# Optimization experiments

Hardware: AMD Instinct MI355X
Metric: run time of the kernel (lower is better)

## Reference

```python
import jax, jax.numpy as jnp
import numpy as np
from jax import lax

GROUPS = 8
THR = 0.5
EPS = 1e-5

def setup_inputs() -> dict:
    key = jax.random.key(0)
    ks = jax.random.split(key, 7)
    b, c, h, w = 64, 256, 1024, 1
    cg = c // GROUPS  # 32
    x = jax.random.normal(ks[0], (b, c, h, w), jnp.float32)
    w1 = jax.random.normal(ks[1], (cg, cg), jnp.float32) * 0.1     # conv1x1 weight [out,in]
    b1 = jnp.zeros((cg,), jnp.float32)
    w3 = jax.random.normal(ks[2], (cg, cg, 3, 3), jnp.float32) * 0.05  # conv3x3 OIHW
    b3 = jnp.zeros((cg,), jnp.float32)
    gamma = jnp.ones((cg,), jnp.float32)
    beta = jnp.zeros((cg,), jnp.float32)
    return {"x": x, "w1": w1, "b1": b1, "w3": w3, "b3": b3, "gamma": gamma, "beta": beta}

def reference(x, w1, b1, w3, b3, gamma, beta):
    b, c, h, w = x.shape
    g = GROUPS
    cg = c // g
    bg = b * g
    gx = x.reshape(bg, cg, h, w)

    # pool_h is AvgPool2d((1,1)) -> identity; pool_w averages over h then permutes
    x_h = gx                                               # [bg,cg,h,1]
    x_w = jnp.mean(gx, axis=2, keepdims=True).transpose(0, 1, 3, 2)  # [bg,cg,w,1]
    cat = jnp.concatenate([x_h, x_w], axis=2)              # [bg,cg,h+w,1]
    hw = jnp.einsum('oi,bihw->bohw', w1, cat) + b1[None, :, None, None]
    xh, xw = hw[:, :, :h], hw[:, :, h:]                    # [bg,cg,h,1], [bg,cg,w,1]

    gated = gx * jax.nn.sigmoid(xh) * jax.nn.sigmoid(xw.transpose(0, 1, 3, 2))
    # GroupNorm(cg, cg): normalize each channel over spatial dims, affine per channel
    mu = jnp.mean(gated, axis=(2, 3), keepdims=True)
    var = jnp.mean(jnp.square(gated - mu), axis=(2, 3), keepdims=True)
    x1 = (gated - mu) * lax.rsqrt(var + EPS) * gamma[None, :, None, None] + beta[None, :, None, None]

    x2 = lax.conv_general_dilated(gx, w3, (1, 1), ((1, 1), (1, 1)),
                                  dimension_numbers=('NCHW', 'OIHW', 'NCHW')) + b3[None, :, None, None]

    # agp: AvgPool2d((avg_len,1)) with h==avg_len, w==1 -> mean over spatial dims
    x11 = jax.nn.softmax(jnp.mean(x1, axis=(2, 3)), axis=-1)  # [bg,cg]
    x21 = jax.nn.softmax(jnp.mean(x2, axis=(2, 3)), axis=-1)  # [bg,cg]
    x12 = x2.reshape(bg, cg, h * w)
    x22 = x1.reshape(bg, cg, h * w)
    weights = (jnp.einsum('bc,bcn->bn', x11, x12) +
               jnp.einsum('bc,bcn->bn', x21, x22)).reshape(bg, 1, h, w)

    rew = gx * jax.nn.sigmoid(weights)
    info = rew >= THR
    x_1 = jnp.where(info, gx, 0.0)
    x_2 = jnp.where(info, 0.0, gx)
    half = cg // 2
    out = jnp.concatenate([x_1[:, :half] + x_2[:, half:],
                           x_1[:, half:] + x_2[:, :half]], axis=1)
    return out.reshape(b, c, h, w)
```

## Files before the change

### kernel.cpp

```cpp
#include <hip/hip_runtime.h>
#include <math.h>

#define CG   32
#define H    1024
#define NBG  512
#define CHN  8
#define BROW (H + 2)
#define EPSV 1e-5f
#define THRV 0.5f

__global__ __launch_bounds__(1024, 4)
void emaru_kernel(const float* __restrict__ x,  const float* __restrict__ w1,
                  const float* __restrict__ b1, const float* __restrict__ w3,
                  const float* __restrict__ b3, const float* __restrict__ gamma,
                  const float* __restrict__ beta, float* __restrict__ out)
{
    __shared__ float  buf[CHN][BROW];
    __shared__ float  w1s[1024];
    __shared__ float  w3s[3072];
    __shared__ double redP[CG][2];
    __shared__ double redQ[CG][2];
    __shared__ float  sigwS[CG], x11S[CG], x21S[CG], As[CG], Bs[CG], Cs[CG],
                      muS[CG], rsgS[CG], b1S[CG], b3S[CG], betaS[CG],
                      g0S[CG], gNS[CG];

    const int t  = threadIdx.x;
    const int bg = blockIdx.x;
    const long base = (long)bg * (CG * H);
    const int wid = t >> 6, lane = t & 63;

    w1s[t] = w1[t];
    #pragma unroll
    for (int r = 0; r < 3; ++r) w3s[r*1024 + t] = w3[(r*1024 + t)*3 + 1];
    if (t < CG) { b1S[t] = b1[t]; b3S[t] = b3[t]; betaS[t] = beta[t]; }

    float g[CG], gated[CG];
    #pragma unroll
    for (int c = 0; c < CG; ++c) g[c] = x[base + c*H + t];
    if (t == 0) {
        #pragma unroll
        for (int c = 0; c < CG; ++c) g0S[c] = g[c];
    }
    if (t == H-1) {
        #pragma unroll
        for (int c = 0; c < CG; ++c) gNS[c] = g[c];
    }
    __syncthreads();

    if (t < CG) {
        float m = betaS[0];
        #pragma unroll
        for (int i = 1; i < CG; ++i) m = fmaxf(m, betaS[i]);
        float s = 0.f;
        #pragma unroll
        for (int i = 0; i < CG; ++i) s += expf(betaS[i] - m);
        const float inv = 1.f / s;
        x11S[t] = expf(betaS[t] - m) * inv;
        float a = 0.f, b = 0.f, c = 0.f;
        #pragma unroll
        for (int o = 0; o < CG; ++o) {
            const float f = expf(betaS[o] - m) * inv;
            a = fmaf(f, w3s[(o*CG + t)*3 + 0], a);
            b = fmaf(f, w3s[(o*CG + t)*3 + 1], b);
            c = fmaf(f, w3s[(o*CG + t)*3 + 2], c);
        }
        As[t] = a; Bs[t] = b; Cs[t] = c;
    }

    float cd = 0.f;
    #pragma unroll
    for (int ch = 0; ch < CG/CHN; ++ch) {
        __syncthreads();
        #pragma unroll
        for (int i = 0; i < CHN; ++i) buf[i][1 + t] = g[ch*CHN + i];
        if (t < CHN) { buf[t][0] = 0.f; buf[t][1 + H] = 0.f; }
        __syncthreads();
        {
            const int cl = wid >> 1, half = wid & 1;
            const int pos = half*512 + lane;
            double acc = 0.0;
            #pragma unroll
            for (int k = 0; k < 8; ++k) acc += (double)buf[cl][1 + pos + (k << 6)];
            #pragma unroll
            for (int off = 32; off; off >>= 1) acc += __shfl_down(acc, off);
            if (lane == 0) redP[ch*CHN + cl][half] = acc;
        }
        #pragma unroll
        for (int i = 0; i < CHN; ++i) {
            const int gi = ch*CHN + i;
            cd = fmaf(As[gi], buf[i][t],     cd);
            cd = fmaf(Bs[gi], g[gi],         cd);
            cd = fmaf(Cs[gi], buf[i][2 + t], cd);
        }
    }
    __syncthreads();

    if (wid == 0 && lane < CG) {
        const int o = lane;
        float acc = b1S[o];
        for (int i = 0; i < CG; ++i) {
            const float mi = (float)((redP[i][0] + redP[i][1]) * (1.0/H));
            acc = fmaf(w1s[o*CG + i], mi, acc);
        }
        sigwS[o] = 1.f / (1.f + expf(-acc));
    } else if (wid == 1 && lane < CG) {
        const int o = lane;
        double m2 = 0.0;
        for (int i = 0; i < CG; ++i) {
            const double Si = redP[i][0] + redP[i][1];
            m2 += (double)w3s[(o*CG + i)*3 + 0] * (Si - (double)gNS[i])
                + (double)w3s[(o*CG + i)*3 + 1] * Si
                + (double)w3s[(o*CG + i)*3 + 2] * (Si - (double)g0S[i]);
        }
        float mv = (float)(m2 * (1.0/H)) + b3S[o];
        float mx = mv;
        #pragma unroll
        for (int off = 16; off; off >>= 1) mx = fmaxf(mx, __shfl_xor(mx, off));
        const float e = expf(mv - mx);
        float se = e;
        #pragma unroll
        for (int off = 16; off; off >>= 1) se += __shfl_xor(se, off);
        x21S[o] = e / se;
    }
    __syncthreads();

    #pragma unroll
    for (int o = 0; o < CG; ++o) {
        float acc = b1S[o];
        #pragma unroll
        for (int i4 = 0; i4 < CG/4; ++i4) {
            const float4 wv = *reinterpret_cast<const float4*>(&w1s[o*CG + i4*4]);
            acc = fmaf(wv.x, g[i4*4+0], acc);
            acc = fmaf(wv.y, g[i4*4+1], acc);
            acc = fmaf(wv.z, g[i4*4+2], acc);
            acc = fmaf(wv.w, g[i4*4+3], acc);
        }
        gated[o] = g[o] * (1.f / (1.f + expf(-acc))) * sigwS[o];
    }
    #pragma unroll
    for (int o = 0; o < CG; ++o) cd = fmaf(x11S[o], b3S[o], cd);

    #pragma unroll
    for (int ch = 0; ch < CG/CHN; ++ch) {
        __syncthreads();
        #pragma unroll
        for (int i = 0; i < CHN; ++i) buf[i][1 + t] = gated[ch*CHN + i];
        __syncthreads();
        const int cl = wid >> 1, half = wid & 1;
        const int pos = half*512 + lane;
        double sg = 0.0, sq = 0.0;
        #pragma unroll
        for (int k = 0; k < 8; ++k) {
            const double v = (double)buf[cl][1 + pos + (k << 6)];
            sg += v; sq = fma(v, v, sq);
        }
        #pragma unroll
        for (int off = 32; off; off >>= 1) { sg += __shfl_down(sg, off); sq += __shfl_down(sq, off); }
        if (lane == 0) { redP[ch*CHN + cl][half] = sg; redQ[ch*CHN + cl][half] = sq; }
    }
    __syncthreads();
    if (t < CG) {
        const double sg = redP[t][0] + redP[t][1];
        const double sq = redQ[t][0] + redQ[t][1];
        const double mu  = sg * (1.0/H);
        const double var = sq * (1.0/H) - mu*mu;
        muS[t]  = (float)mu;
        rsgS[t] = (float)(1.0 / sqrt(var + (double)EPSV)) * gamma[t];
    }
    __syncthreads();

    float wsum = cd;
    #pragma unroll
    for (int o = 0; o < CG; ++o) {
        const float x1o = fmaf(gated[o] - muS[o], rsgS[o], betaS[o]);
        wsum = fmaf(x21S[o], x1o, wsum);
    }
    const float s = 1.f / (1.f + expf(-wsum));
    #pragma unroll
    for (int o = 0; o < CG/2; ++o) {
        const float ga = g[o], gb = g[o + CG/2];
        const bool ia = (ga * s) >= THRV;
        const bool ib = (gb * s) >= THRV;
        out[base + o*H + t]          = (ia ? ga : 0.f) + (ib ? 0.f : gb);
        out[base + (o + CG/2)*H + t] = (ib ? gb : 0.f) + (ia ? 0.f : ga);
    }
}

extern "C" void kernel_launch(void* const* d_in, const int* in_sizes, int n_in,
                              void* d_out, int out_size, void* d_ws, size_t ws_size,
                              hipStream_t stream) {
    const float* x     = (const float*)d_in[0];
    const float* w1    = (const float*)d_in[1];
    const float* b1    = (const float*)d_in[2];
    const float* w3    = (const float*)d_in[3];
    const float* b3    = (const float*)d_in[4];
    const float* gamma = (const float*)d_in[5];
    const float* beta  = (const float*)d_in[6];
    float* out = (float*)d_out;
    emaru_kernel<<<NBG, 1024, 0, stream>>>(x, w1, b1, w3, b3, gamma, beta, out);
}
```

Baseline: 358.5 us.

## Compute gated values per chunk to drop the gated register array

```diff
diff --git a/kernel.cpp b/kernel.cpp
--- a/kernel.cpp
+++ b/kernel.cpp
@@ -9,7 +9,8 @@
 #define EPSV 1e-5f
 #define THRV 0.5f
 
-__global__ __launch_bounds__(1024, 4)
+__global__ __launch_bounds__(1024)
+__attribute__((amdgpu_waves_per_eu(4, 4)))
 void emaru_kernel(const float* __restrict__ x,  const float* __restrict__ w1,
                   const float* __restrict__ b1, const float* __restrict__ w3,
                   const float* __restrict__ b3, const float* __restrict__ gamma,
@@ -18,11 +19,10 @@
     __shared__ float  buf[CHN][BROW];
     __shared__ float  w1s[1024];
     __shared__ float  w3s[3072];
-    __shared__ double redP[CG][2];
-    __shared__ double redQ[CG][2];
+    __shared__ double sumS[CG];
     __shared__ float  sigwS[CG], x11S[CG], x21S[CG], As[CG], Bs[CG], Cs[CG],
                       muS[CG], rsgS[CG], b1S[CG], b3S[CG], betaS[CG],
-                      g0S[CG], gNS[CG];
+                      g0S[CG], gNS[CG], gammaS[CG];
 
     const int t  = threadIdx.x;
     const int bg = blockIdx.x;
@@ -32,9 +32,9 @@
     w1s[t] = w1[t];
     #pragma unroll
     for (int r = 0; r < 3; ++r) w3s[r*1024 + t] = w3[(r*1024 + t)*3 + 1];
-    if (t < CG) { b1S[t] = b1[t]; b3S[t] = b3[t]; betaS[t] = beta[t]; }
+    if (t < CG) { b1S[t] = b1[t]; b3S[t] = b3[t]; betaS[t] = beta[t]; gammaS[t] = gamma[t]; }
 
-    float g[CG], gated[CG];
+    float g[CG];
     #pragma unroll
     for (int c = 0; c < CG; ++c) g[c] = x[base + c*H + t];
     if (t == 0) {
@@ -75,15 +75,13 @@
         for (int i = 0; i < CHN; ++i) buf[i][1 + t] = g[ch*CHN + i];
         if (t < CHN) { buf[t][0] = 0.f; buf[t][1 + H] = 0.f; }
         __syncthreads();
-        {
-            const int cl = wid >> 1, half = wid & 1;
-            const int pos = half*512 + lane;
+        if (wid < CHN) {
             double acc = 0.0;
             #pragma unroll
-            for (int k = 0; k < 8; ++k) acc += (double)buf[cl][1 + pos + (k << 6)];
+            for (int k = 0; k < 16; ++k) acc += (double)buf[wid][1 + lane + (k << 6)];
             #pragma unroll
             for (int off = 32; off; off >>= 1) acc += __shfl_down(acc, off);
-            if (lane == 0) redP[ch*CHN + cl][half] = acc;
+            if (lane == 0) sumS[ch*CHN + wid] = acc;
         }
         #pragma unroll
         for (int i = 0; i < CHN; ++i) {
@@ -99,7 +97,7 @@
         const int o = lane;
         float acc = b1S[o];
         for (int i = 0; i < CG; ++i) {
-            const float mi = (float)((redP[i][0] + redP[i][1]) * (1.0/H));
+            const float mi = (float)(sumS[i] * (1.0/H));
             acc = fmaf(w1s[o*CG + i], mi, acc);
         }
         sigwS[o] = 1.f / (1.f + expf(-acc));
@@ -107,7 +105,7 @@
         const int o = lane;
         double m2 = 0.0;
         for (int i = 0; i < CG; ++i) {
-            const double Si = redP[i][0] + redP[i][1];
+            const double Si = sumS[i];
             m2 += (double)w3s[(o*CG + i)*3 + 0] * (Si - (double)gNS[i])
                 + (double)w3s[(o*CG + i)*3 + 1] * Si
                 + (double)w3s[(o*CG + i)*3 + 2] * (Si - (double)g0S[i]);
@@ -125,56 +123,52 @@
     __syncthreads();
 
     #pragma unroll
-    for (int o = 0; o < CG; ++o) {
-        float acc = b1S[o];
-        #pragma unroll
-        for (int i4 = 0; i4 < CG/4; ++i4) {
-            const float4 wv = *reinterpret_cast<const float4*>(&w1s[o*CG + i4*4]);
-            acc = fmaf(wv.x, g[i4*4+0], acc);
-            acc = fmaf(wv.y, g[i4*4+1], acc);
-            acc = fmaf(wv.z, g[i4*4+2], acc);
-            acc = fmaf(wv.w, g[i4*4+3], acc);
-        }
-        gated[o] = g[o] * (1.f / (1.f + expf(-acc))) * sigwS[o];
-    }
-    #pragma unroll
     for (int o = 0; o < CG; ++o) cd = fmaf(x11S[o], b3S[o], cd);
-
+    float wsum = cd;
     #pragma unroll
     for (int ch = 0; ch < CG/CHN; ++ch) {
         __syncthreads();
         #pragma unroll
-        for (int i = 0; i < CHN; ++i) buf[i][1 + t] = gated[ch*CHN + i];
+        for (int i = 0; i < CHN; ++i) {
+            const int o = ch*CHN + i;
+            float acc = b1S[o];
+            #pragma unroll
+            for (int i4 = 0; i4 < CG/4; ++i4) {
+                const float4 wv = *reinterpret_cast<const float4*>(&w1s[o*CG + i4*4]);
+                acc = fmaf(wv.x, g[i4*4+0], acc);
+                acc = fmaf(wv.y, g[i4*4+1], acc);
+                acc = fmaf(wv.z, g[i4*4+2], acc);
+                acc = fmaf(wv.w, g[i4*4+3], acc);
+            }
+            buf[i][1 + t] = g[o] * (1.f / (1.f + expf(-acc))) * sigwS[o];
+        }
         __syncthreads();
-        const int cl = wid >> 1, half = wid & 1;
-        const int pos = half*512 + lane;
-        double sg = 0.0, sq = 0.0;
+        if (wid < CHN) {
+            double sg = 0.0, sq = 0.0;
+            #pragma unroll
+            for (int k = 0; k < 16; ++k) {
+                const double v = (double)buf[wid][1 + lane + (k << 6)];
+                sg += v; sq = fma(v, v, sq);
+            }
+            #pragma unroll
+            for (int off = 32; off; off >>= 1) { sg += __shfl_down(sg, off); sq += __shfl_down(sq, off); }
+            if (lane == 0) {
+                const int o = ch*CHN + wid;
+                const double mu  = sg * (1.0/H);
+                const double var = sq * (1.0/H) - mu*mu;
+                muS[o]  = (float)mu;
+                rsgS[o] = (float)(1.0 / sqrt(var + (double)EPSV)) * gammaS[o];
+            }
+        }
+        __syncthreads();
         #pragma unroll
-        for (int k = 0; k < 8; ++k) {
-            const double v = (double)buf[cl][1 + pos + (k << 6)];
-            sg += v; sq = fma(v, v, sq);
+        for (int i = 0; i < CHN; ++i) {
+            const int o = ch*CHN + i;
+            const float x1o = fmaf(buf[i][1 + t] - muS[o], rsgS[o], betaS[o]);
+            wsum = fmaf(x21S[o], x1o, wsum);
         }
-        #pragma unroll
-        for (int off = 32; off; off >>= 1) { sg += __shfl_down(sg, off); sq += __shfl_down(sq, off); }
-        if (lane == 0) { redP[ch*CHN + cl][half] = sg; redQ[ch*CHN + cl][half] = sq; }
     }
-    __syncthreads();
-    if (t < CG) {
-        const double sg = redP[t][0] + redP[t][1];
-        const double sq = redQ[t][0] + redQ[t][1];
-        const double mu  = sg * (1.0/H);
-        const double var = sq * (1.0/H) - mu*mu;
-        muS[t]  = (float)mu;
-        rsgS[t] = (float)(1.0 / sqrt(var + (double)EPSV)) * gamma[t];
-    }
-    __syncthreads();
 
-    float wsum = cd;
-    #pragma unroll
-    for (int o = 0; o < CG; ++o) {
-        const float x1o = fmaf(gated[o] - muS[o], rsgS[o], betaS[o]);
-        wsum = fmaf(x21S[o], x1o, wsum);
-    }
     const float s = 1.f / (1.f + expf(-wsum));
     #pragma unroll
     for (int o = 0; o < CG/2; ++o) {
```

After: 396.7 us. +10.7%, slower.
